# Optimization experiments

Measured on AMD Instinct MI355X. Metric: run time of the kernel, lower is better.

Reference implementation:

```python
import jax, jax.numpy as jnp
import numpy as np

B, T, D, C = 4, 8192, 1024, 64  # batch, seq_len, d_model, chunk_size


def setup_inputs() -> dict:
    key = jax.random.key(0)
    k1, k2, k3 = jax.random.split(key, 3)
    out = jax.random.normal(k1, (B, T, D), jnp.float32)
    W_write = jax.random.normal(k2, (D, D), jnp.float32) / np.float32(np.sqrt(D))
    W_read = jax.random.normal(k3, (D, D), jnp.float32) / np.float32(np.sqrt(D))
    decay = jnp.float32(4.6)                     # torch init: tensor(4.6)
    log_alpha = jnp.log(jnp.float32(0.03))       # torch init: log(memory_alpha)
    return {"out": out, "W_write": W_write, "W_read": W_read,
            "decay": decay, "log_alpha": log_alpha}


def reference(out, W_write, W_read, decay, log_alpha):
    Bd, Td, Dd = out.shape
    nC = Td // C  # T chosen divisible by chunk_size
    out32 = out.astype(jnp.float32)
    gamma = jax.nn.sigmoid(decay)
    log_gamma = jnp.log(gamma)

    v = out32 @ W_write.T                               # proj_write
    wk = jnp.pad(out32[:, :-1], ((0, 0), (1, 0), (0, 0)))  # shift right by 1
    rk = out32

    p = jnp.arange(C)
    diffs = jnp.maximum(p[:, None] - 1 - p[None, :], 0)
    causal = (p[:, None] > p[None, :]).astype(jnp.float32)
    M = jnp.exp(diffs * log_gamma) * causal             # (C, C) intra-chunk decay mask
    dec_inter = gamma ** p                              # (C,)
    gw = gamma ** (C - 1 - p)                           # (C,)
    gC = gamma ** C

    def chunk(x):  # (B,T,D) -> (nC,B,C,D) for scan over chunks
        return x.reshape(Bd, nC, C, Dd).transpose(1, 0, 2, 3)

    rk_c, wk_c, v_c = chunk(rk), chunk(wk), chunk(v)

    def body(W, xs):
        r, w, vv = xs                                   # each (B,C,D)
        inter = jnp.einsum('bde,bce->bcd', W, r) * dec_inter[None, :, None]
        S = jnp.einsum('bcd,bed->bce', r, w)            # (B,C,C)
        intra = jnp.einsum('bce,bed->bcd', S * M, vv)
        W_new = gC * W + jnp.einsum('bcd,bce->bde', vv * gw[None, :, None], w)
        return W_new, inter + intra

    W0 = jnp.zeros((Bd, Dd, Dd), jnp.float32)
    _, reads = jax.lax.scan(body, W0, (rk_c, wk_c, v_c))  # reads: (nC,B,C,D)
    reads = reads.transpose(1, 0, 2, 3).reshape(Bd, Td, Dd)

    alpha = jnp.exp(log_alpha)
    return out + alpha * (reads @ W_read.T).astype(out.dtype)
```

## Files before the change

kernel.cpp:

```cpp
#include <hip/hip_runtime.h>


typedef __attribute__((ext_vector_type(8))) short short8;
typedef __attribute__((ext_vector_type(4))) short short4v;
typedef __attribute__((ext_vector_type(4))) float f32x4;

#define B_ 4
#define T_ 8192
#define D_ 1024
#define C_ 64
#define NC_ 128
#define CHS_ 64

#define DEVI static __device__ __forceinline__

#define EXPF(x) __builtin_expf(x)
#define LOG2F(x) __builtin_log2f(x)
#define EXP2F(x) __builtin_exp2f(x)

DEVI unsigned short f2bf_u(float f) {
  unsigned int u = __float_as_uint(f);
  u += 0x7fffu + ((u >> 16) & 1u);
  return (unsigned short)(u >> 16);
}
DEVI short f2bfs(float f) { return (short)f2bf_u(f); }
DEVI float bf2fs(short h) { return __uint_as_float(((unsigned int)(unsigned short)h) << 16); }

DEVI f32x4 mfma16(short8 a, short8 b, f32x4 c) {
  return __builtin_amdgcn_mfma_f32_16x16x32_bf16(a, b, c, 0, 0, 0);
}

DEVI void chunk_barrier() {
  asm volatile("s_waitcnt lgkmcnt(0)" ::: "memory");
  __builtin_amdgcn_s_barrier();
}

__global__ __launch_bounds__(256) void k_cast(const float* __restrict__ src,
                                              short* __restrict__ dst, int n8) {
  int i = blockIdx.x * 256 + threadIdx.x;
  if (i >= n8) return;
  const float4* s = (const float4*)src;
  float4 a = s[2 * i], b = s[2 * i + 1];
  short8 o;
  o[0] = f2bfs(a.x); o[1] = f2bfs(a.y); o[2] = f2bfs(a.z); o[3] = f2bfs(a.w);
  o[4] = f2bfs(b.x); o[5] = f2bfs(b.y); o[6] = f2bfs(b.z); o[7] = f2bfs(b.w);
  *((short8*)dst + i) = o;
}

__global__ __launch_bounds__(256) void k_transT(const short* __restrict__ rk,
                                                short* __restrict__ wTg) {
  __shared__ short ts[64][72];
  const int tid = threadIdx.x;
  const int t0 = blockIdx.x * 64, e0 = blockIdx.y * 64, b = blockIdx.z;
  const short* rk_b = rk + (size_t)b * T_ * D_;
  short* w_b = wTg + (size_t)b * D_ * T_;
  const int lr = tid >> 3, ls = tid & 7;
#pragma unroll
  for (int p = 0; p < 2; ++p) {
    int row = p * 32 + lr;
    int t = t0 - 1 + row;
    short8 v8;
    if (t >= 0) v8 = *(const short8*)(rk_b + (size_t)t * D_ + e0 + ls * 8);
    else v8 = (short8){0, 0, 0, 0, 0, 0, 0, 0};
    *(short8*)&ts[row][ls * 8] = v8;
  }
  __syncthreads();
  const int er5 = tid & 31, thi = tid >> 5;
#pragma unroll
  for (int ep = 0; ep < 2; ++ep) {
    int erow = ep * 32 + er5;
    short8 w8;
#pragma unroll
    for (int j = 0; j < 8; ++j) w8[j] = ts[thi * 8 + j][erow];
    *(short8*)(w_b + (size_t)(e0 + erow) * T_ + t0 + thi * 8) = w8;
  }
}

__global__ __launch_bounds__(256) void k_gemm_v(const short* __restrict__ Aw,
                                                const short* __restrict__ Bx,
                                                short* __restrict__ vT) {
  __shared__ short As[128][72];
  __shared__ short Bs[128][72];
  const int tid = threadIdx.x;
  const int lane = tid & 63, wv = tid >> 6;
  const int wm = (wv >> 1) * 64, wn = (wv & 1) * 64;
  const int l16 = lane & 15, q = lane >> 4;
  const int m0 = blockIdx.y * 128;
  const int n0 = blockIdx.x * 128;
  f32x4 acc[4][4];
  for (int a = 0; a < 4; ++a)
    for (int b = 0; b < 4; ++b) acc[a][b] = (f32x4){0.f, 0.f, 0.f, 0.f};
  const int lrow = tid >> 3, lseg = tid & 7;
  const short* Ap = Aw + (size_t)(m0 + lrow) * D_ + lseg * 8;
  const short* Bp = Bx + (size_t)(n0 + lrow) * D_ + lseg * 8;
  for (int kb = 0; kb < D_; kb += 64) {
#pragma unroll
    for (int p = 0; p < 4; ++p) {
      *(short8*)&As[lrow + p * 32][lseg * 8] = *(const short8*)(Ap + (size_t)(p * 32) * D_ + kb);
      *(short8*)&Bs[lrow + p * 32][lseg * 8] = *(const short8*)(Bp + (size_t)(p * 32) * D_ + kb);
    }
    __syncthreads();
#pragma unroll
    for (int ks = 0; ks < 2; ++ks) {
      short8 af[4], bfr[4];
#pragma unroll
      for (int mt = 0; mt < 4; ++mt) af[mt] = *(const short8*)&As[wm + mt * 16 + l16][ks * 32 + q * 8];
#pragma unroll
      for (int nt = 0; nt < 4; ++nt) bfr[nt] = *(const short8*)&Bs[wn + nt * 16 + l16][ks * 32 + q * 8];
#pragma unroll
      for (int mt = 0; mt < 4; ++mt)
#pragma unroll
        for (int nt = 0; nt < 4; ++nt) acc[mt][nt] = mfma16(af[mt], bfr[nt], acc[mt][nt]);
    }
    __syncthreads();
  }
  const int b = n0 >> 13;
  const int tbase = (n0 & (T_ - 1)) + wn;
  short* outp = vT + (size_t)b * D_ * T_;
#pragma unroll
  for (int mt = 0; mt < 4; ++mt)
#pragma unroll
    for (int nt = 0; nt < 4; ++nt)
#pragma unroll
      for (int i = 0; i < 4; ++i) {
        int d = m0 + wm + mt * 16 + q * 4 + i;
        int t = tbase + nt * 16 + l16;
        outp[(size_t)d * T_ + t] = f2bfs(acc[mt][nt][i]);
      }
}

__global__ __launch_bounds__(1024, 4) void k_scan(const short* __restrict__ rk,
                                                  const short* __restrict__ vT_g,
                                                  const short* __restrict__ wTg,
                                                  short* __restrict__ inter_,
                                                  short* __restrict__ Sg,
                                                  const float* __restrict__ decay_p) {
  __shared__ short rs[2][64][128];
  __shared__ short wTs_[2][128][64];
  __shared__ short Wb[32][1024];
  __shared__ short vTs[32][72];
  __shared__ float red[2][64][36];

  const int tid = threadIdx.x;
  const int lane = tid & 63;
  const int wv = tid >> 6;
  const int l16 = lane & 15, q = lane >> 4;
  const int dt = blockIdx.x, b = blockIdx.y, sg = blockIdx.z;
  const int d0 = dt * 32;
  const int tseg0 = sg * (CHS_ * 64);
  const float gamma = 1.f / (1.f + EXPF(-decay_p[0]));
  const float lg2g = LOG2F(gamma);
  const float gC = EXP2F(64.f * lg2g);

  const short* rk_b = rk + (size_t)b * T_ * D_;
  const short* wT_b = wTg + (size_t)b * D_ * T_;
  const short* vT_b = vT_g + (size_t)b * D_ * T_;

  const int dsub = wv >> 3, ct = (wv >> 1) & 3, krp = wv & 1;
  const int dh = wv >> 3, et = wv & 7;
  const int l7 = l16 & 7;

  const int arow = tid >> 4, aunit = tid & 15;
  const int wrow = tid >> 3, wunit = tid & 7;
  const short* aG = rk_b + (size_t)(tseg0 + arow) * D_ + aunit * 8;
  const short* wG = wT_b + (size_t)wrow * T_ + tseg0 + wunit * 8;
  const int asw = (aunit ^ (arow & 7)) * 8;
  const int wsw = (wunit ^ (wrow & 7)) * 8;

  const bool vrole = (tid >= 512);
  const int vd = (tid - 512) >> 4;
  const int vc4 = ((tid - 512) & 15) << 2;
  const short* vptr = vT_b + (size_t)(d0 + vd) * T_ + tseg0 + vc4;
  short4v vpre;

  f32x4 Wacc[8];
#pragma unroll
  for (int j = 0; j < 8; ++j) Wacc[j] = (f32x4){0.f, 0.f, 0.f, 0.f};
  f32x4 iacc = (f32x4){0.f, 0.f, 0.f, 0.f};

  short8 pfA, pfW;
  auto issue = [&](int g2) {
    int nch = g2 >> 3, ns = g2 & 7;
    pfA = *(const short8*)(aG + (size_t)(nch * 64) * D_ + ns * 128);
    pfW = *(const short8*)(wG + (size_t)(ns * 128) * T_ + nch * 64);
  };
  auto write_pf = [&](int buf) {
    *(short8*)&rs[buf][arow][asw] = pfA;
    *(short8*)&wTs_[buf][wrow][wsw] = pfW;
  };
  auto write_vTs = [&]() {
#pragma unroll
    for (int j = 0; j < 4; ++j)
      vTs[vd][vc4 + j] = f2bfs(bf2fs(vpre[j]) * EXP2F(lg2g * (float)(63 - (vc4 + j))));
  };

  issue(0);
  if (vrole) vpre = *(const short4v*)vptr;
  write_pf(0);
  if (vrole) write_vTs();
  {
    short4v z4 = (short4v){0, 0, 0, 0};
#pragma unroll
    for (int i = 0; i < 8; ++i) ((short4v*)&Wb[0][0])[tid + i * 1024] = z4;
  }
  issue(1);
  __syncthreads();

  short8 a2k0, a2k1;
  for (int ch = 0; ch < CHS_; ++ch) {
#pragma unroll
    for (int s = 0; s < 8; ++s) {
      const int g = ch * 8 + s;
      const int cur = s & 1;
      if (s == 0) {
        a2k0 = *(const short8*)&vTs[dh * 16 + l16][q * 8];
        a2k1 = *(const short8*)&vTs[dh * 16 + l16][32 + q * 8];
        if (vrole) {
          int chn = (ch + 1 < CHS_) ? ch + 1 : ch;
          vpre = *(const short4v*)(vptr + chn * 64);
        }
      }
      if (g + 1 < CHS_ * 8) write_pf((s + 1) & 1);
      if (g + 2 < CHS_ * 8) issue(g + 2);
#pragma unroll
      for (int u = 0; u < 2; ++u) {
        int kr = krp * 2 + u;
        short8 af = *(const short8*)&rs[cur][ct * 16 + l16][((kr * 4 + q) ^ l7) * 8];
        short8 bfr = *(const short8*)&Wb[dsub * 16 + l16][((s * 16 + kr * 4 + q) ^ l7) * 8];
        iacc = mfma16(bfr, af, iacc);
      }
      {
        short8 bw0 = *(const short8*)&wTs_[cur][et * 16 + l16][(q ^ l7) * 8];
        short8 bw1 = *(const short8*)&wTs_[cur][et * 16 + l16][((4 + q) ^ l7) * 8];
        Wacc[s] = mfma16(bw0, a2k0, Wacc[s]);
        Wacc[s] = mfma16(bw1, a2k1, Wacc[s]);
      }
      chunk_barrier();
    }
    *(f32x4*)&red[krp][ct * 16 + l16][dsub * 16 + q * 4] = iacc;
    iacc = (f32x4){0.f, 0.f, 0.f, 0.f};
    {
      const int row_d = dh * 16 + l16;
#pragma unroll
      for (int s2 = 0; s2 < 8; ++s2) {
        short4v w4;
#pragma unroll
        for (int i = 0; i < 4; ++i) w4[i] = f2bfs(Wacc[s2][i]);
        int e_base = s2 * 128 + et * 16 + q * 4;
        int unit = e_base >> 3;
        *(short4v*)&Wb[row_d][((unit ^ l7) << 3) + (e_base & 7)] = w4;
        if (sg == 0 && ch == CHS_ - 1)
          *(short4v*)(Sg + ((size_t)b * D_ + d0 + row_d) * D_ + e_base) = w4;
#pragma unroll
        for (int i = 0; i < 4; ++i) Wacc[s2][i] *= gC;
      }
    }
    if (vrole && ch + 1 < CHS_) write_vTs();
    chunk_barrier();
    if (tid < 256) {
      int c = tid >> 2, dq = tid & 3;
      f32x4 s0 = *(const f32x4*)&red[0][c][dq * 8];
      f32x4 s1 = *(const f32x4*)&red[0][c][dq * 8 + 4];
      s0 += *(const f32x4*)&red[1][c][dq * 8];
      s1 += *(const f32x4*)&red[1][c][dq * 8 + 4];
      float sc = EXP2F(lg2g * (float)c);
      short8 o;
#pragma unroll
      for (int i = 0; i < 4; ++i) { o[i] = f2bfs(s0[i] * sc); o[4 + i] = f2bfs(s1[i] * sc); }
      *(short8*)(inter_ + (size_t)b * T_ * D_ +
                 (size_t)(tseg0 + ch * 64 + c) * D_ + d0 + dq * 8) = o;
    }
  }
}

__global__ __launch_bounds__(256) void k_corr(const short* __restrict__ rk,
                                              const short* __restrict__ Sg,
                                              short* __restrict__ inter_,
                                              const float* __restrict__ decay_p) {
  __shared__ short As[128][72];
  __shared__ short Bs[128][72];
  const int tid = threadIdx.x;
  const int lane = tid & 63, wv = tid >> 6;
  const int wm = (wv >> 1) * 64, wn = (wv & 1) * 64;
  const int l16 = lane & 15, q = lane >> 4;
  const int m0 = blockIdx.x * 128;
  const int n0 = blockIdx.y * 128;
  const int b = blockIdx.z;
  const float gamma = 1.f / (1.f + EXPF(-decay_p[0]));
  const float lg2g = LOG2F(gamma);
  const short* Ab = rk + (size_t)b * T_ * D_ + (size_t)(4096 + m0) * D_;
  const short* Bb = Sg + (size_t)b * D_ * D_ + (size_t)n0 * D_;
  f32x4 acc[4][4];
  for (int a = 0; a < 4; ++a)
    for (int c = 0; c < 4; ++c) acc[a][c] = (f32x4){0.f, 0.f, 0.f, 0.f};
  const int lrow = tid >> 3, lseg = tid & 7;
  for (int kb = 0; kb < D_; kb += 64) {
#pragma unroll
    for (int p = 0; p < 4; ++p) {
      *(short8*)&As[lrow + p * 32][lseg * 8] =
          *(const short8*)(Ab + (size_t)(lrow + p * 32) * D_ + kb + lseg * 8);
      *(short8*)&Bs[lrow + p * 32][lseg * 8] =
          *(const short8*)(Bb + (size_t)(lrow + p * 32) * D_ + kb + lseg * 8);
    }
    __syncthreads();
#pragma unroll
    for (int ks = 0; ks < 2; ++ks) {
      short8 af[4], bfr[4];
#pragma unroll
      for (int mt = 0; mt < 4; ++mt) af[mt] = *(const short8*)&As[wm + mt * 16 + l16][ks * 32 + q * 8];
#pragma unroll
      for (int nt = 0; nt < 4; ++nt) bfr[nt] = *(const short8*)&Bs[wn + nt * 16 + l16][ks * 32 + q * 8];
#pragma unroll
      for (int mt = 0; mt < 4; ++mt)
#pragma unroll
        for (int nt = 0; nt < 4; ++nt) acc[mt][nt] = mfma16(af[mt], bfr[nt], acc[mt][nt]);
    }
    __syncthreads();
  }
#pragma unroll
  for (int mt = 0; mt < 4; ++mt)
#pragma unroll
    for (int nt = 0; nt < 4; ++nt)
#pragma unroll
      for (int i = 0; i < 4; ++i) {
        int lt = m0 + wm + mt * 16 + q * 4 + i;
        int d = n0 + wn + nt * 16 + l16;
        size_t idx = (size_t)b * T_ * D_ + (size_t)(4096 + lt) * D_ + d;
        float cur = bf2fs(inter_[idx]);
        inter_[idx] = f2bfs(cur + acc[mt][nt][i] * EXP2F(lg2g * (float)lt));
      }
}

__global__ __launch_bounds__(256) void k_intra(const short* __restrict__ rk,
                                               const short* __restrict__ vT_g,
                                               short* __restrict__ intra_,
                                               const float* __restrict__ decay_p) {
  __shared__ short rs[65][264];
  __shared__ short P[64][72];
  __shared__ short vs[256][72];
  const int tid = threadIdx.x;
  const int lane = tid & 63, wv = tid >> 6;
  const int l16 = lane & 15, q = lane >> 4;
  const int ch = blockIdx.x, b = blockIdx.y;
  const int t0 = ch << 6;
  const float gamma = 1.f / (1.f + EXPF(-decay_p[0]));
  const float lg2g = LOG2F(gamma);
  const short* rk_b = rk + (size_t)b * T_ * D_;
  f32x4 Sacc[4];
#pragma unroll
  for (int j = 0; j < 4; ++j) Sacc[j] = (f32x4){0.f, 0.f, 0.f, 0.f};

  for (int s = 0; s < 4; ++s) {
    const int e0 = s << 8;
#pragma unroll
    for (int p = 0; p < 9; ++p) {
      int idx = p * 256 + tid;
      if (idx < 2080) {
        int row = idx >> 5, seg = idx & 31;
        int t = t0 - 1 + row;
        short8 v8;
        if (t >= 0) v8 = *(const short8*)(rk_b + (size_t)t * D_ + e0 + seg * 8);
        else v8 = (short8){0, 0, 0, 0, 0, 0, 0, 0};
        *(short8*)&rs[row][seg * 8] = v8;
      }
    }
    __syncthreads();
#pragma unroll
    for (int ks = 0; ks < 8; ++ks) {
      short8 af = *(const short8*)&rs[wv * 16 + l16 + 1][ks * 32 + q * 8];
#pragma unroll
      for (int nt = 0; nt < 4; ++nt) {
        short8 bfr = *(const short8*)&rs[nt * 16 + l16][ks * 32 + q * 8];
        Sacc[nt] = mfma16(af, bfr, Sacc[nt]);
      }
    }
    __syncthreads();
  }
#pragma unroll
  for (int nt = 0; nt < 4; ++nt)
#pragma unroll
    for (int i = 0; i < 4; ++i) {
      int c = wv * 16 + q * 4 + i;
      int cp = nt * 16 + l16;
      float m = (c > cp) ? EXP2F(lg2g * (float)(c - 1 - cp)) : 0.f;
      P[c][cp] = f2bfs(Sacc[nt][i] * m);
    }
  __syncthreads();
  const short* vsrc = vT_g + (size_t)b * D_ * T_ + (size_t)tid * T_ + t0;
  size_t base = (size_t)b * T_ * D_;
  for (int p = 0; p < 4; ++p) {
    const short* sp = vsrc + (size_t)(p * 256) * T_;
#pragma unroll
    for (int seg = 0; seg < 8; ++seg)
      *(short8*)&vs[tid][seg * 8] = *(const short8*)(sp + seg * 8);
    __syncthreads();
    f32x4 acc[4][4];
#pragma unroll
    for (int a = 0; a < 4; ++a)
#pragma unroll
      for (int bb = 0; bb < 4; ++bb) acc[a][bb] = (f32x4){0.f, 0.f, 0.f, 0.f};
#pragma unroll
    for (int ks2 = 0; ks2 < 2; ++ks2) {
      short8 af[4];
#pragma unroll
      for (int mt = 0; mt < 4; ++mt) af[mt] = *(const short8*)&P[mt * 16 + l16][ks2 * 32 + q * 8];
#pragma unroll
      for (int nt = 0; nt < 4; ++nt) {
        short8 bfr = *(const short8*)&vs[wv * 64 + nt * 16 + l16][ks2 * 32 + q * 8];
#pragma unroll
        for (int mt = 0; mt < 4; ++mt) acc[mt][nt] = mfma16(af[mt], bfr, acc[mt][nt]);
      }
    }
#pragma unroll
    for (int mt = 0; mt < 4; ++mt)
#pragma unroll
      for (int nt = 0; nt < 4; ++nt)
#pragma unroll
        for (int i = 0; i < 4; ++i) {
          int c = mt * 16 + q * 4 + i;
          int d = p * 256 + wv * 64 + nt * 16 + l16;
          intra_[base + (size_t)(t0 + c) * D_ + d] = f2bfs(acc[mt][nt][i]);
        }
    __syncthreads();
  }
}

__global__ __launch_bounds__(256) void k_gemm_final(const short* __restrict__ inter_,
                                                    const short* __restrict__ intra_,
                                                    const short* __restrict__ Wr,
                                                    const float* __restrict__ xin,
                                                    float* __restrict__ y,
                                                    const float* __restrict__ la_p) {
  __shared__ short As[128][72];
  __shared__ short Bs[128][72];
  const float alpha = EXPF(la_p[0]);
  const int tid = threadIdx.x;
  const int lane = tid & 63, wv = tid >> 6;
  const int wm = (wv >> 1) * 64, wn = (wv & 1) * 64;
  const int l16 = lane & 15, q = lane >> 4;
  const int m0 = blockIdx.x * 128;
  const int n0 = blockIdx.y * 128;
  f32x4 acc[4][4];
  for (int a = 0; a < 4; ++a)
    for (int b = 0; b < 4; ++b) acc[a][b] = (f32x4){0.f, 0.f, 0.f, 0.f};
  const int lrow = tid >> 3, lseg = tid & 7;
  for (int kb = 0; kb < D_; kb += 64) {
#pragma unroll
    for (int p = 0; p < 4; ++p) {
      size_t aoff = (size_t)(m0 + lrow + p * 32) * D_ + kb + lseg * 8;
      short8 xa = *(const short8*)(inter_ + aoff);
      short8 xb = *(const short8*)(intra_ + aoff);
      short8 xs;
#pragma unroll
      for (int j = 0; j < 8; ++j) xs[j] = f2bfs(bf2fs(xa[j]) + bf2fs(xb[j]));
      *(short8*)&As[lrow + p * 32][lseg * 8] = xs;
      *(short8*)&Bs[lrow + p * 32][lseg * 8] =
          *(const short8*)(Wr + (size_t)(n0 + lrow + p * 32) * D_ + kb + lseg * 8);
    }
    __syncthreads();
#pragma unroll
    for (int ks = 0; ks < 2; ++ks) {
      short8 af[4], bfr[4];
#pragma unroll
      for (int mt = 0; mt < 4; ++mt) af[mt] = *(const short8*)&As[wm + mt * 16 + l16][ks * 32 + q * 8];
#pragma unroll
      for (int nt = 0; nt < 4; ++nt) bfr[nt] = *(const short8*)&Bs[wn + nt * 16 + l16][ks * 32 + q * 8];
#pragma unroll
      for (int mt = 0; mt < 4; ++mt)
#pragma unroll
        for (int nt = 0; nt < 4; ++nt) acc[mt][nt] = mfma16(af[mt], bfr[nt], acc[mt][nt]);
    }
    __syncthreads();
  }
#pragma unroll
  for (int mt = 0; mt < 4; ++mt)
#pragma unroll
    for (int nt = 0; nt < 4; ++nt)
#pragma unroll
      for (int i = 0; i < 4; ++i) {
        int t = m0 + wm + mt * 16 + q * 4 + i;
        int d = n0 + wn + nt * 16 + l16;
        size_t idx = (size_t)t * D_ + d;
        y[idx] = xin[idx] + alpha * acc[mt][nt][i];
      }
}

extern "C" void kernel_launch(void* const* d_in, const int* in_sizes, int n_in,
                              void* d_out, int out_size, void* d_ws, size_t ws_size,
                              hipStream_t stream) {
  const float* x = (const float*)d_in[0];
  const float* Ww = (const float*)d_in[1];
  const float* Wr = (const float*)d_in[2];
  const float* decay = (const float*)d_in[3];
  const float* log_alpha = (const float*)d_in[4];
  float* y = (float*)d_out;

  short* ws = (short*)d_ws;
  const size_t NTD = (size_t)B_ * T_ * D_;
  short* rk_bf = ws;
  short* vT_bf = rk_bf + NTD;
  short* inter_b = vT_bf + NTD;
  short* intra_b = inter_b + NTD;
  short* Ww_bf = intra_b + NTD;
  short* Wr_bf = Ww_bf + (size_t)D_ * D_;
  short* Sg = Wr_bf + (size_t)D_ * D_;
  short* wTg = intra_b;

  k_cast<<<(int)(NTD / 8 / 256), 256, 0, stream>>>(x, rk_bf, (int)(NTD / 8));
  k_cast<<<512, 256, 0, stream>>>(Ww, Ww_bf, (D_ * D_) / 8);
  k_cast<<<512, 256, 0, stream>>>(Wr, Wr_bf, (D_ * D_) / 8);
  k_transT<<<dim3(T_ / 64, D_ / 64, B_), 256, 0, stream>>>(rk_bf, wTg);
  k_gemm_v<<<dim3(256, 8), 256, 0, stream>>>(Ww_bf, rk_bf, vT_bf);
  k_scan<<<dim3(32, 4, 2), 1024, 0, stream>>>(rk_bf, vT_bf, wTg, inter_b, Sg, decay);
  k_corr<<<dim3(16, 8, 4), 256, 0, stream>>>(rk_bf, Sg, inter_b, decay);
  k_intra<<<dim3(128, 4), 256, 0, stream>>>(rk_bf, vT_bf, intra_b, decay);
  k_gemm_final<<<dim3(256, 8), 256, 0, stream>>>(inter_b, intra_b, Wr_bf, x, y, log_alpha);
}
```

Baseline: 941.2 us.

## Load scan rk fragments directly from global into registers, dropping LDS staging

The inter-chunk read in the scan kernel no longer stages rk tiles through a double-buffered shared-memory array. Each wave now loads its MFMA A-fragments straight from global memory into registers, using ping-pong register sets prefetched one step ahead. The wave split is remapped so each wave covers two c-tiles over one k-slice, which doubles the accumulators and grows the cross-wave reduction buffer from 2 to 4 partials. This saves LDS capacity and LDS write/read traffic, at the cost of uncoalesced per-lane global loads, more redundant rk fetches across waves, and extra register pressure.

```diff
diff --git a/kernel.cpp b/kernel.cpp
--- a/kernel.cpp
+++ b/kernel.cpp
@@ -135,11 +135,10 @@
                                                   short* __restrict__ inter_,
                                                   short* __restrict__ Sg,
                                                   const float* __restrict__ decay_p) {
-  __shared__ short rs[2][64][128];
   __shared__ short wTs_[2][128][64];
   __shared__ short Wb[32][1024];
   __shared__ short vTs[32][72];
-  __shared__ float red[2][64][36];
+  __shared__ float red[4][64][36];
 
   const int tid = threadIdx.x;
   const int lane = tid & 63;
@@ -156,16 +155,15 @@
   const short* wT_b = wTg + (size_t)b * D_ * T_;
   const short* vT_b = vT_g + (size_t)b * D_ * T_;
 
-  const int dsub = wv >> 3, ct = (wv >> 1) & 3, krp = wv & 1;
+  const int dsub = wv >> 3, ctp = (wv >> 2) & 1, kr = wv & 3;
   const int dh = wv >> 3, et = wv & 7;
   const int l7 = l16 & 7;
 
-  const int arow = tid >> 4, aunit = tid & 15;
   const int wrow = tid >> 3, wunit = tid & 7;
-  const short* aG = rk_b + (size_t)(tseg0 + arow) * D_ + aunit * 8;
   const short* wG = wT_b + (size_t)wrow * T_ + tseg0 + wunit * 8;
-  const int asw = (aunit ^ (arow & 7)) * 8;
   const int wsw = (wunit ^ (wrow & 7)) * 8;
+
+  const short* afb = rk_b + (size_t)(tseg0 + ctp * 32 + l16) * D_ + kr * 32 + q * 8;
 
   const bool vrole = (tid >= 512);
   const int vd = (tid - 512) >> 4;
@@ -176,17 +174,30 @@
   f32x4 Wacc[8];
 #pragma unroll
   for (int j = 0; j < 8; ++j) Wacc[j] = (f32x4){0.f, 0.f, 0.f, 0.f};
-  f32x4 iacc = (f32x4){0.f, 0.f, 0.f, 0.f};
-
-  short8 pfA, pfW;
-  auto issue = [&](int g2) {
+  f32x4 iacc[2];
+  iacc[0] = (f32x4){0.f, 0.f, 0.f, 0.f};
+  iacc[1] = (f32x4){0.f, 0.f, 0.f, 0.f};
+
+  short8 pfW;
+  auto issue_w = [&](int g2) {
     int nch = g2 >> 3, ns = g2 & 7;
-    pfA = *(const short8*)(aG + (size_t)(nch * 64) * D_ + ns * 128);
     pfW = *(const short8*)(wG + (size_t)(ns * 128) * T_ + nch * 64);
   };
-  auto write_pf = [&](int buf) {
-    *(short8*)&rs[buf][arow][asw] = pfA;
+  auto write_w = [&](int buf) {
     *(short8*)&wTs_[buf][wrow][wsw] = pfW;
+  };
+  short8 afE0, afE1, afO0, afO1;
+  auto issue_afE = [&](int g2) {
+    int nch = g2 >> 3, ns = g2 & 7;
+    const short* p = afb + (size_t)(nch * 64) * D_ + ns * 128;
+    afE0 = *(const short8*)p;
+    afE1 = *(const short8*)(p + (size_t)16 * D_);
+  };
+  auto issue_afO = [&](int g2) {
+    int nch = g2 >> 3, ns = g2 & 7;
+    const short* p = afb + (size_t)(nch * 64) * D_ + ns * 128;
+    afO0 = *(const short8*)p;
+    afO1 = *(const short8*)(p + (size_t)16 * D_);
   };
   auto write_vTs = [&]() {
 #pragma unroll
@@ -194,16 +205,17 @@
       vTs[vd][vc4 + j] = f2bfs(bf2fs(vpre[j]) * EXP2F(lg2g * (float)(63 - (vc4 + j))));
   };
 
-  issue(0);
+  issue_w(0);
+  issue_afE(0);
   if (vrole) vpre = *(const short4v*)vptr;
-  write_pf(0);
+  write_w(0);
   if (vrole) write_vTs();
   {
     short4v z4 = (short4v){0, 0, 0, 0};
 #pragma unroll
     for (int i = 0; i < 8; ++i) ((short4v*)&Wb[0][0])[tid + i * 1024] = z4;
   }
-  issue(1);
+  issue_w(1);
   __syncthreads();
 
   short8 a2k0, a2k1;
@@ -220,14 +232,21 @@
           vpre = *(const short4v*)(vptr + chn * 64);
         }
       }
-      if (g + 1 < CHS_ * 8) write_pf((s + 1) & 1);
-      if (g + 2 < CHS_ * 8) issue(g + 2);
-#pragma unroll
-      for (int u = 0; u < 2; ++u) {
-        int kr = krp * 2 + u;
-        short8 af = *(const short8*)&rs[cur][ct * 16 + l16][((kr * 4 + q) ^ l7) * 8];
+      if (g + 1 < CHS_ * 8) write_w((s + 1) & 1);
+      if (g + 2 < CHS_ * 8) issue_w(g + 2);
+      if (g + 1 < CHS_ * 8) {
+        if ((s & 1) == 0) issue_afO(g + 1);
+        else issue_afE(g + 1);
+      }
+      {
         short8 bfr = *(const short8*)&Wb[dsub * 16 + l16][((s * 16 + kr * 4 + q) ^ l7) * 8];
-        iacc = mfma16(bfr, af, iacc);
+        if ((s & 1) == 0) {
+          iacc[0] = mfma16(bfr, afE0, iacc[0]);
+          iacc[1] = mfma16(bfr, afE1, iacc[1]);
+        } else {
+          iacc[0] = mfma16(bfr, afO0, iacc[0]);
+          iacc[1] = mfma16(bfr, afO1, iacc[1]);
+        }
       }
       {
         short8 bw0 = *(const short8*)&wTs_[cur][et * 16 + l16][(q ^ l7) * 8];
@@ -237,8 +256,10 @@
       }
       chunk_barrier();
     }
-    *(f32x4*)&red[krp][ct * 16 + l16][dsub * 16 + q * 4] = iacc;
-    iacc = (f32x4){0.f, 0.f, 0.f, 0.f};
+    *(f32x4*)&red[kr][(ctp * 2) * 16 + l16][dsub * 16 + q * 4] = iacc[0];
+    *(f32x4*)&red[kr][(ctp * 2 + 1) * 16 + l16][dsub * 16 + q * 4] = iacc[1];
+    iacc[0] = (f32x4){0.f, 0.f, 0.f, 0.f};
+    iacc[1] = (f32x4){0.f, 0.f, 0.f, 0.f};
     {
       const int row_d = dh * 16 + l16;
 #pragma unroll
@@ -261,8 +282,11 @@
       int c = tid >> 2, dq = tid & 3;
       f32x4 s0 = *(const f32x4*)&red[0][c][dq * 8];
       f32x4 s1 = *(const f32x4*)&red[0][c][dq * 8 + 4];
-      s0 += *(const f32x4*)&red[1][c][dq * 8];
-      s1 += *(const f32x4*)&red[1][c][dq * 8 + 4];
+#pragma unroll
+      for (int p = 1; p < 4; ++p) {
+        s0 += *(const f32x4*)&red[p][c][dq * 8];
+        s1 += *(const f32x4*)&red[p][c][dq * 8 + 4];
+      }
       float sc = EXP2F(lg2g * (float)c);
       short8 o;
 #pragma unroll
```

New measurement: 1.148 ms. 21.9% more time.
